# Performance work log

Measured on AMD Instinct MI355X. Metric: run time of the kernel, lower is better.

The kernel has to match this reference:

```python
import jax, jax.numpy as jnp
import numpy as np

NEG_INF = -1e32

def _linear(x, W, b):
    # torch nn.Linear: x @ W.T + b
    return x @ W.T + b

def setup_inputs() -> dict:
    key = jax.random.key(0)
    B, T, D, H = 8, 1024, 512, 8
    ks = jax.random.split(key, 16)
    def rn(i, shape, scale=1.0):
        return jax.random.normal(ks[i], shape, dtype=jnp.float32) * scale
    W_SCALE = 0.04  # ~xavier for 512x512
    inp = {
        'q_mean': rn(0, (B, T, D)), 'q_cov': rn(1, (B, T, D)),
        'k_mean': rn(2, (B, T, D)), 'k_cov': rn(3, (B, T, D)),
        'v_mean': rn(4, (B, T, D)), 'v_cov': rn(5, (B, T, D)),
        # kq_same=True: q projections share k weights
        'Wk_mean': rn(6, (D, D), W_SCALE), 'bk_mean': jnp.zeros((D,), jnp.float32),
        'Wk_cov':  rn(7, (D, D), W_SCALE), 'bk_cov':  jnp.zeros((D,), jnp.float32),
        'Wv_mean': rn(8, (D, D), W_SCALE), 'bv_mean': jnp.zeros((D,), jnp.float32),
        'Wv_cov':  rn(9, (D, D), W_SCALE), 'bv_cov':  jnp.zeros((D,), jnp.float32),
        'Wo_mean': rn(10, (D, D), W_SCALE), 'bo_mean': jnp.zeros((D,), jnp.float32),
        'Wo_cov':  rn(11, (D, D), W_SCALE), 'bo_cov':  jnp.zeros((D,), jnp.float32),
        'gammas': rn(12, (H, 1, 1), 0.3),
        'mask': jnp.broadcast_to(jnp.tril(jnp.ones((T, T), dtype=bool))[None, None], (B, 1, T, T)),
        'zero_pad': 1,
    }
    return inp

def reference(q_mean, q_cov, k_mean, k_cov, v_mean, v_cov,
              Wk_mean, bk_mean, Wk_cov, bk_cov,
              Wv_mean, bv_mean, Wv_cov, bv_cov,
              Wo_mean, bo_mean, Wo_cov, bo_cov,
              gammas, mask, zero_pad):
    B, T, D = q_mean.shape
    H = gammas.shape[0]
    dk = D // H
    def split(x):  # (B,T,D) -> (B,H,T,dk)
        return x.reshape(B, T, H, dk).transpose(0, 2, 1, 3)
    km = split(_linear(k_mean, Wk_mean, bk_mean))
    kc = split(_linear(k_cov,  Wk_cov,  bk_cov))
    qm = split(_linear(q_mean, Wk_mean, bk_mean))  # kq_same
    qc = split(_linear(q_cov,  Wk_cov,  bk_cov))
    vm = split(_linear(v_mean, Wv_mean, bv_mean))
    vc = split(_linear(v_cov,  Wv_cov,  bv_cov))

    # Wasserstein distance (B,H,T,T)
    m1sq = jnp.sum(qm ** 2, -1, keepdims=True)
    m2sq = jnp.sum(km ** 2, -1, keepdims=True)
    ret = -2.0 * jnp.einsum('bhtd,bhsd->bhts', qm, km) + m1sq + jnp.swapaxes(m2sq, -1, -2)
    sq_q = jnp.sqrt(jnp.clip(qc, 1e-24))
    sq_k = jnp.sqrt(jnp.clip(kc, 1e-24))
    cov_ret = (-2.0 * jnp.einsum('bhtd,bhsd->bhts', sq_q, sq_k)
               + jnp.sum(qc, -1, keepdims=True)
               + jnp.swapaxes(jnp.sum(kc, -1, keepdims=True), -1, -2))
    scores = -(ret + cov_ret) / jnp.sqrt(jnp.float32(dk))

    # cumulative position-decay term (no-grad block in torch)
    s_ = jnp.where(mask, scores, NEG_INF)
    s_ = jax.nn.softmax(s_, axis=-1) * mask.astype(scores.dtype)
    distcum = jnp.cumsum(s_, axis=-1)
    disttot = jnp.sum(s_, axis=-1, keepdims=True)
    idx = jnp.arange(T)
    pos = jnp.abs(idx[None, :] - idx[:, None]).astype(jnp.float32)[None, None]  # (1,1,T,T)
    dist_scores = jax.lax.stop_gradient(jnp.sqrt(jnp.clip((disttot - distcum) * pos, 0.0)))

    gamma = -jax.nn.softplus(gammas)[None]  # (1,H,1,1)
    total_effect = jnp.clip(jnp.exp(dist_scores * gamma), 1e-5, 1e5)
    scores = jnp.where(mask, scores * total_effect, NEG_INF)
    scores = jax.nn.softmax(scores, axis=-1)
    if zero_pad:
        scores = scores.at[:, :, 0, :].set(0.0)
    # dropout is identity (p=0 / eval)

    out_mean = jnp.einsum('bhts,bhsd->bhtd', scores, vm)
    out_cov  = jnp.einsum('bhts,bhsd->bhtd', scores ** 2, vc)
    cm = out_mean.transpose(0, 2, 1, 3).reshape(B, T, D)
    cc = out_cov.transpose(0, 2, 1, 3).reshape(B, T, D)
    return (_linear(cm, Wo_mean, bo_mean), _linear(cc, Wo_cov, bo_cov))
```

## Files before the change

kernel.cpp:

```cpp
#include <hip/hip_runtime.h>
#include <hip/hip_bf16.h>
#include <hip/hip_fp16.h>

#define Bb 8
#define Tt 1024
#define Dd 512
#define Hh 8

typedef _Float16 half8 __attribute__((ext_vector_type(8)));
typedef float floatx4 __attribute__((ext_vector_type(4)));

__device__ __forceinline__ half8 cvt8(float4 a, float4 b) {
    half8 h;
    h[0] = (_Float16)a.x; h[1] = (_Float16)a.y; h[2] = (_Float16)a.z; h[3] = (_Float16)a.w;
    h[4] = (_Float16)b.x; h[5] = (_Float16)b.y; h[6] = (_Float16)b.z; h[7] = (_Float16)b.w;
    return h;
}

__device__ __forceinline__ void async16(const _Float16* g, _Float16* l) {
    __builtin_amdgcn_global_load_lds(
        (const __attribute__((address_space(1))) uint32_t*)g,
        (__attribute__((address_space(3))) uint32_t*)l, 16, 0, 0);
}

#define DPP_ADD(v, ctrl) \
    ((v) + __int_as_float(__builtin_amdgcn_update_dpp(0, __float_as_int(v), (ctrl), 0xF, 0xF, true)))

__device__ __forceinline__ float red16(float v) {
    v = DPP_ADD(v, 0xB1);
    v = DPP_ADD(v, 0x4E);
    v = DPP_ADD(v, 0x141);
    v = DPP_ADD(v, 0x140);
    return v;
}
__device__ __forceinline__ float scan16(float v) {
    v = DPP_ADD(v, 0x111);
    v = DPP_ADD(v, 0x112);
    v = DPP_ADD(v, 0x114);
    v = DPP_ADD(v, 0x118);
    return v;
}

__global__ __launch_bounds__(256) void cvt_pre(
    const float* __restrict__ s0, const float* __restrict__ s1,
    const float* __restrict__ s2, const float* __restrict__ s3,
    const float* __restrict__ s4, const float* __restrict__ s5,
    const float* __restrict__ w0, const float* __restrict__ w1,
    const float* __restrict__ w2, const float* __restrict__ w3,
    const float* __restrict__ w4, const float* __restrict__ w5,
    _Float16* __restrict__ dst)
{
    const size_t N_BTD = (size_t)Bb * Tt * Dd;
    const size_t NX = 6 * N_BTD;
    const size_t total8 = (NX + 6 * 262144) / 8;
    size_t i = (size_t)blockIdx.x * 256 + threadIdx.x;
    const size_t stride = (size_t)gridDim.x * 256;
    for (; i < total8; i += stride) {
        const size_t e = i * 8;
        const float* src;
        size_t off;
        if (e < NX) {
            const int seg = (int)(e >> 22);
            off = e & (N_BTD - 1);
            src = (seg == 0) ? s0 : (seg == 1) ? s1 : (seg == 2) ? s2
                : (seg == 3) ? s3 : (seg == 4) ? s4 : s5;
        } else {
            const size_t we = e - NX;
            const int seg = (int)(we >> 18);
            off = we & 262143;
            src = (seg == 0) ? w0 : (seg == 1) ? w1 : (seg == 2) ? w2
                : (seg == 3) ? w3 : (seg == 4) ? w4 : w5;
        }
        float4 a = *(const float4*)(src + off);
        float4 b = *(const float4*)(src + off + 4);
        *(half8*)(dst + e) = cvt8(a, b);
    }
}

template<bool TR>
__device__ __forceinline__ void gemm_tile_h(
    const _Float16* __restrict__ X, const _Float16* __restrict__ W,
    _Float16* As, _Float16* Bs, int m0, int n0, floatx4 acc[8])
{
    const int tid = threadIdx.x;
    const int w = tid >> 6, lane = tid & 63;
    const int sl = lane & 15, quad = lane >> 4;
    const int j7 = tid & 7;
    const int swz = sl & 7;

    for (int k0 = 0; k0 < 512; k0 += 64) {
        #pragma unroll
        for (int i = 0; i < 2; i++) {
            const int slot = i * 256 + tid;
            const int row = slot >> 3;
            async16(X + (size_t)(m0 + row) * 512 + k0 + ((j7 ^ (row & 7)) << 3),
                    As + slot * 8);
        }
        #pragma unroll
        for (int i = 0; i < 4; i++) {
            const int slot = i * 256 + tid;
            const int row = slot >> 3;
            async16(W + (size_t)(n0 + row) * 512 + k0 + ((j7 ^ (row & 7)) << 3),
                    Bs + slot * 8);
        }
        __syncthreads();
        #pragma unroll
        for (int kc = 0; kc < 64; kc += 32) {
            const int jq = (kc >> 3) + quad;
            const half8 af = *(const half8*)(As + (w * 16 + sl) * 64 + ((jq ^ swz) << 3));
            #pragma unroll
            for (int tn = 0; tn < 8; tn++) {
                const half8 bf = *(const half8*)(Bs + (tn * 16 + sl) * 64 + ((jq ^ swz) << 3));
                if constexpr (TR)
                    acc[tn] = __builtin_amdgcn_mfma_f32_16x16x32_f16(bf, af, acc[tn], 0, 0, 0);
                else
                    acc[tn] = __builtin_amdgcn_mfma_f32_16x16x32_f16(af, bf, acc[tn], 0, 0, 0);
            }
        }
        __syncthreads();
    }
}

__global__ __launch_bounds__(256) void gemm6(
    const _Float16* __restrict__ XH, const _Float16* __restrict__ WH,
    const float* __restrict__ bk_mean, const float* __restrict__ bk_cov,
    const float* __restrict__ bv_mean, const float* __restrict__ bv_cov,
    _Float16* __restrict__ QB, _Float16* __restrict__ KB, _Float16* __restrict__ VB,
    float* __restrict__ RROW, float* __restrict__ CCOL)
{
    __shared__ __align__(16) _Float16 As[64 * 64];
    __shared__ __align__(16) _Float16 Bs[128 * 64];

    const int f = blockIdx.x;
    const int work = (f & 7) * 384 + (f >> 3);
    const int z = work >> 9;
    const int rem = work & 511;
    const int m0 = (rem >> 2) * 64;
    const int n0 = (rem & 3) * 128;

    const size_t N_BTD = (size_t)Bb * Tt * Dd;
    const _Float16* X = XH + (size_t)z * N_BTD;
    const _Float16* W;
    const float* bias;
    _Float16* outH; float* sums;
    int off, sumsq, do_sqrt;
    switch (z) {
    case 0:  W=WH;            bias=bk_mean; outH=QB; sums=RROW;   off=0;  sumsq=1; do_sqrt=0; break;
    case 1:  W=WH+262144;     bias=bk_cov;  outH=QB; sums=RROW;   off=64; sumsq=0; do_sqrt=1; break;
    case 2:  W=WH;            bias=bk_mean; outH=KB; sums=CCOL;   off=0;  sumsq=1; do_sqrt=0; break;
    case 3:  W=WH+262144;     bias=bk_cov;  outH=KB; sums=CCOL;   off=64; sumsq=0; do_sqrt=1; break;
    case 4:  W=WH+2*262144;   bias=bv_mean; outH=VB; sums=nullptr;off=0;  sumsq=0; do_sqrt=0; break;
    default: W=WH+3*262144;   bias=bv_cov;  outH=VB; sums=nullptr;off=64; sumsq=0; do_sqrt=0; break;
    }

    floatx4 acc[8];
    #pragma unroll
    for (int tn = 0; tn < 8; tn++) acc[tn] = (floatx4){0.f, 0.f, 0.f, 0.f};

    const int tid = threadIdx.x;
    const int w = tid >> 6, lane = tid & 63;
    const int sl = lane & 15, quad = lane >> 4;

    if (z < 4) {
        gemm_tile_h<false>(X, W, As, Bs, m0, n0, acc);
        #pragma unroll
        for (int r = 0; r < 4; r++) {
            const int m = m0 + w * 16 + quad * 4 + r;
            const int b = m >> 10, t = m & 1023;
            float rs0 = 0.f, rs1 = 0.f;
            #pragma unroll
            for (int tn = 0; tn < 8; tn++) {
                const int n = n0 + tn * 16 + sl;
                const float v = acc[tn][r] + bias[n];
                if (tn < 4) rs0 += sumsq ? v * v : v;
                else        rs1 += sumsq ? v * v : v;
                const float sv = do_sqrt ? sqrtf(fmaxf(v, 1e-24f)) : v;
                const int head = n >> 6, dd = n & 63;
                outH[(((size_t)b * Hh + head) * Tt + t) * 128 + off + dd] = (_Float16)sv;
            }
            if (sums) {
                float v0 = rs0, v1 = rs1;
                v0 += __shfl_xor(v0, 1); v0 += __shfl_xor(v0, 2);
                v0 += __shfl_xor(v0, 4); v0 += __shfl_xor(v0, 8);
                v1 += __shfl_xor(v1, 1); v1 += __shfl_xor(v1, 2);
                v1 += __shfl_xor(v1, 4); v1 += __shfl_xor(v1, 8);
                if (sl == 0) {
                    atomicAdd(&sums[((size_t)b * Hh + (n0 >> 6) + 0) * Tt + t], v0);
                    atomicAdd(&sums[((size_t)b * Hh + (n0 >> 6) + 1) * Tt + t], v1);
                }
            }
        }
    } else {
        gemm_tile_h<true>(X, W, As, Bs, m0, n0, acc);
        const int m = m0 + w * 16 + sl;
        const int b = m >> 10, t = m & 1023;
        #pragma unroll
        for (int r = 0; r < 4; r++) {
            #pragma unroll
            for (int tn = 0; tn < 8; tn++) {
                const int n = n0 + tn * 16 + quad * 4 + r;
                const float v = acc[tn][r] + bias[n];
                const int head = n >> 6, dd = n & 63;
                outH[(((size_t)b * Hh + head) * 128 + off + dd) * 1024 + t] = (_Float16)v;
            }
        }
    }
}

__global__ __launch_bounds__(256) void gemm_out(
    const _Float16* __restrict__ CMh, const _Float16* __restrict__ CCh,
    const _Float16* __restrict__ WH,
    const float* __restrict__ bo_mean, const float* __restrict__ bo_cov,
    float* __restrict__ out, size_t outStride)
{
    __shared__ __align__(16) _Float16 As[64 * 64];
    __shared__ __align__(16) _Float16 Bs[128 * 64];

    const int f = blockIdx.x;
    const int work = (f & 7) * 128 + (f >> 3);
    const int z = work >> 9;
    const int rem = work & 511;
    const int m0 = (rem >> 2) * 64;
    const int n0 = (rem & 3) * 128;

    const _Float16* X = z ? CCh : CMh;
    const _Float16* W = WH + (size_t)(4 + z) * 262144;
    const float* bias = z ? bo_cov : bo_mean;
    float* outF       = out + (size_t)z * outStride;

    floatx4 acc[8];
    #pragma unroll
    for (int tn = 0; tn < 8; tn++) acc[tn] = (floatx4){0.f, 0.f, 0.f, 0.f};
    gemm_tile_h<false>(X, W, As, Bs, m0, n0, acc);

    const int tid = threadIdx.x;
    const int w = tid >> 6, lane = tid & 63;
    const int sl = lane & 15, quad = lane >> 4;

    #pragma unroll
    for (int r = 0; r < 4; r++) {
        const int m = m0 + w * 16 + quad * 4 + r;
        #pragma unroll
        for (int tn = 0; tn < 8; tn++) {
            const int n = n0 + tn * 16 + sl;
            outF[(size_t)m * 512 + n] = acc[tn][r] + bias[n];
        }
    }
}

__global__ __launch_bounds__(256) void pass_a(
    const _Float16* __restrict__ QB, const _Float16* __restrict__ KB,
    const float* __restrict__ RROW, const float* __restrict__ CCOL,
    float* __restrict__ L1)
{
    const int tri = blockIdx.x;
    int rt = (int)((sqrtf(8.f * (float)tri + 1.f) - 1.f) * 0.5f);
    while ((rt + 1) * (rt + 2) / 2 <= tri) rt++;
    while (rt * (rt + 1) / 2 > tri) rt--;
    const int c = tri - rt * (rt + 1) / 2;
    const int bh = blockIdx.y;

    const int tid = threadIdx.x;
    const int w = tid >> 6, lane = tid & 63;
    const int sl = lane & 15, quad = lane >> 4;
    const int t0 = rt * 64;
    const int tbase = t0 + w * 16 + quad * 4;
    const size_t rowbase = (size_t)bh * Tt;

    half8 af[4];
    {
        const _Float16* qrow = QB + (rowbase + t0 + w * 16 + sl) * 128;
        #pragma unroll
        for (int ks = 0; ks < 4; ks++)
            af[ks] = *(const half8*)(qrow + ks * 32 + quad * 8);
    }
    float rt_[4];
    #pragma unroll
    for (int r = 0; r < 4; r++) rt_[r] = RROW[rowbase + tbase + r];

    const _Float16* KBb = KB + rowbase * 128;
    const float* CCb = CCOL + rowbase;

    float l1p[4] = {0.f, 0.f, 0.f, 0.f};
    #pragma unroll
    for (int su = 0; su < 4; su++) {
        const int scol = c * 64 + su * 16 + sl;
        const _Float16* kr = KBb + (size_t)scol * 128;
        floatx4 acc = {0.f, 0.f, 0.f, 0.f};
        #pragma unroll
        for (int ks = 0; ks < 4; ks++) {
            half8 bf = *(const half8*)(kr + ks * 32 + quad * 8);
            acc = __builtin_amdgcn_mfma_f32_16x16x32_f16(af[ks], bf, acc, 0, 0, 0);
        }
        const float cs = CCb[scol];
        #pragma unroll
        for (int r = 0; r < 4; r++) {
            const float S = 0.25f * acc[r] - 0.125f * (rt_[r] + cs);
            l1p[r] += (scol <= tbase + r) ? __expf(S) : 0.f;
        }
    }
    #pragma unroll
    for (int r = 0; r < 4; r++) {
        const float v = red16(l1p[r]);
        if (sl == 0) atomicAdd(&L1[rowbase + tbase + r], v);
    }
}

__global__ __launch_bounds__(256) void attn_b(
    const _Float16* __restrict__ QB, const _Float16* __restrict__ KB,
    const _Float16* __restrict__ VBt, const float* __restrict__ RROW,
    const float* __restrict__ CCOL, const float* __restrict__ L1,
    const float* __restrict__ gammas, const int* __restrict__ zp,
    _Float16* __restrict__ CMh, _Float16* __restrict__ CCh)
{
    __shared__ __align__(16) _Float16 Vt[2][128 * 64];
    __shared__ __align__(16) _Float16 Pm[4][16 * 64];

    const int tid = threadIdx.x;
    const int g = blockIdx.x >> 6;
    const int bh = blockIdx.x & 63;
    const int rt = (g < 8) ? (15 - g) : (g - 8);
    const int t0 = rt * 64;
    const int h = bh & 7, b = bh >> 3;
    const int w = tid >> 6, lane = tid & 63;
    const int sl = lane & 15, quad = lane >> 4;
    const size_t rowbase = (size_t)bh * Tt;
    const int nch = rt + 1;

    const _Float16* VBb = VBt + (size_t)bh * 128 * 1024;
    const int vr8 = tid >> 3;
    const int vc8 = (tid & 7) << 3;
    const int vswz = (vr8 & 7) << 3;
    const _Float16* vsrc0 = VBb + (size_t)vr8 * 1024 + (vc8 ^ vswz);
    #define STAGE_V(cc, buf) do {                                          \
        const _Float16* _s = vsrc0 + (cc) * 64;                            \
        _Float16* _d = &Vt[(buf)][0] + vr8 * 64 + vc8;                     \
        _Pragma("unroll")                                                  \
        for (int _i = 0; _i < 4; _i++)                                     \
            async16(_s + (size_t)_i * 32 * 1024, _d + _i * 32 * 64);       \
    } while (0)

    STAGE_V(0, 0);

    half8 af[4];
    {
        const _Float16* qrow = QB + (rowbase + t0 + w * 16 + sl) * 128;
        #pragma unroll
        for (int ks = 0; ks < 4; ks++)
            af[ks] = *(const half8*)(qrow + ks * 32 + quad * 8);
    }

    const float gamma = -log1pf(__expf(gammas[h]));
    const int zero_pad = *zp;
    const int tbase = t0 + w * 16 + quad * 4;

    float rt_[4], invl1[4];
    #pragma unroll
    for (int r = 0; r < 4; r++) {
        rt_[r] = RROW[rowbase + tbase + r];
        invl1[r] = 1.f / L1[rowbase + tbase + r];
    }

    const _Float16* KBb = KB + rowbase * 128;
    const float* CCb = CCOL + rowbase;

    __syncthreads();

    float cumc[4] = {0.f, 0.f, 0.f, 0.f};
    float runL2[4] = {0.f, 0.f, 0.f, 0.f};
    floatx4 accm[4], accc[4];
    #pragma unroll
    for (int nt = 0; nt < 4; nt++) {
        accm[nt] = (floatx4){0.f, 0.f, 0.f, 0.f};
        accc[nt] = (floatx4){0.f, 0.f, 0.f, 0.f};
    }
    _Float16* PmW = &Pm[w][0];

    for (int c = 0; c < nch; ++c) {
        const int cur = c & 1;
        if (c + 1 < nch) STAGE_V(c + 1, cur ^ 1);

        float p2v[4][4];
        float csum[4] = {0.f, 0.f, 0.f, 0.f};
        #pragma unroll
        for (int su = 0; su < 4; su++) {
            const int scol = c * 64 + su * 16 + sl;
            const _Float16* kr = KBb + (size_t)scol * 128;
            floatx4 acc = {0.f, 0.f, 0.f, 0.f};
            #pragma unroll
            for (int ks = 0; ks < 4; ks++) {
                half8 bf = *(const half8*)(kr + ks * 32 + quad * 8);
                acc = __builtin_amdgcn_mfma_f32_16x16x32_f16(af[ks], bf, acc, 0, 0, 0);
            }
            const float cs = CCb[scol];
            #pragma unroll
            for (int r = 0; r < 4; r++) {
                const bool valid = (scol <= tbase + r);
                const float S = 0.25f * acc[r] - 0.125f * (rt_[r] + cs);
                const float p1 = valid ? __expf(S) : 0.f;
                const float cum = cumc[r] + scan16(p1);
                cumc[r] += red16(p1);
                const float sn = 1.f - cum * invl1[r];
                const float dsq = sn * (float)(tbase + r - scol);
                const float dist = sqrtf(fmaxf(dsq, 0.f));
                float dec = __expf(gamma * dist);
                dec = fminf(fmaxf(dec, 1e-5f), 1e5f);
                const float p2 = valid ? __expf(S * dec) : 0.f;
                p2v[su][r] = p2;
                csum[r] += p2;
            }
        }

        float invL2c[4];
        #pragma unroll
        for (int r = 0; r < 4; r++) {
            const float v = red16(csum[r]);
            const float newL2 = runL2[r] + v;
            const float inv = 1.f / newL2;
            const float ratio = runL2[r] * inv;
            runL2[r] = newL2;
            invL2c[r] = inv;
            const float ratio2 = ratio * ratio;
            #pragma unroll
            for (int nt = 0; nt < 4; nt++) {
                accm[nt][r] *= ratio;
                accc[nt][r] *= ratio2;
            }
        }
        #pragma unroll
        for (int su = 0; su < 4; su++) {
            #pragma unroll
            for (int r = 0; r < 4; r++) {
                const float pn = p2v[su][r] * invL2c[r];
                const int prow = quad * 4 + r;
                PmW[prow * 64 + ((su * 16 + sl) ^ ((prow & 7) << 3))] = (_Float16)pn;
            }
        }

        const _Float16* Vc = &Vt[cur][0];
        #pragma unroll
        for (int ks = 0; ks < 2; ks++) {
            const int kb = ks * 32 + quad * 8;
            half8 am = *(const half8*)(PmW + sl * 64 + (kb ^ ((sl & 7) << 3)));
            half8 ac = am * am;
            #pragma unroll
            for (int nt = 0; nt < 4; nt++) {
                const int rm = nt * 16 + sl, rc = rm + 64;
                half8 bm = *(const half8*)(Vc + rm * 64 + (kb ^ ((rm & 7) << 3)));
                half8 bc = *(const half8*)(Vc + rc * 64 + (kb ^ ((rc & 7) << 3)));
                accm[nt] = __builtin_amdgcn_mfma_f32_16x16x32_f16(am, bm, accm[nt], 0, 0, 0);
                accc[nt] = __builtin_amdgcn_mfma_f32_16x16x32_f16(ac, bc, accc[nt], 0, 0, 0);
            }
        }
        __syncthreads();
    }

    #pragma unroll
    for (int r = 0; r < 4; r++) {
        const int t = tbase + r;
        const bool zr = (zero_pad && t == 0);
        _Float16* cmp = CMh + ((size_t)b * Tt + t) * Dd + h * 64;
        _Float16* ccp = CCh + ((size_t)b * Tt + t) * Dd + h * 64;
        #pragma unroll
        for (int nt = 0; nt < 4; nt++) {
            const int d = nt * 16 + sl;
            cmp[d] = (_Float16)(zr ? 0.f : accm[nt][r]);
            ccp[d] = (_Float16)(zr ? 0.f : accc[nt][r]);
        }
    }
    #undef STAGE_V
}

extern "C" void kernel_launch(void* const* d_in, const int* in_sizes, int n_in,
                              void* d_out, int out_size, void* d_ws, size_t ws_size,
                              hipStream_t stream)
{
    const float* q_mean  = (const float*)d_in[0];
    const float* q_cov   = (const float*)d_in[1];
    const float* k_mean  = (const float*)d_in[2];
    const float* k_cov   = (const float*)d_in[3];
    const float* v_mean  = (const float*)d_in[4];
    const float* v_cov   = (const float*)d_in[5];
    const float* Wk_mean = (const float*)d_in[6];
    const float* bk_mean = (const float*)d_in[7];
    const float* Wk_cov  = (const float*)d_in[8];
    const float* bk_cov  = (const float*)d_in[9];
    const float* Wv_mean = (const float*)d_in[10];
    const float* bv_mean = (const float*)d_in[11];
    const float* Wv_cov  = (const float*)d_in[12];
    const float* bv_cov  = (const float*)d_in[13];
    const float* Wo_mean = (const float*)d_in[14];
    const float* bo_mean = (const float*)d_in[15];
    const float* Wo_cov  = (const float*)d_in[16];
    const float* bo_cov  = (const float*)d_in[17];
    const float* gammas  = (const float*)d_in[18];
    const int* zero_pad  = (const int*)d_in[20];
    float* out = (float*)d_out;

    const size_t N_BHT128 = (size_t)Bb * Hh * Tt * 128;
    const size_t N_BHT    = (size_t)Bb * Hh * Tt;
    const size_t N_BTD    = (size_t)Bb * Tt * Dd;

    const size_t needed = 3 * N_BHT128 * sizeof(_Float16)
                        + 6 * N_BTD * sizeof(_Float16)
                        + 6 * 262144 * sizeof(_Float16)
                        + 3 * N_BHT * sizeof(float);
    if (ws_size < needed) return;

    _Float16* QB = (_Float16*)d_ws;
    _Float16* KB = QB + N_BHT128;
    _Float16* VB = KB + N_BHT128;
    _Float16* XH = VB + N_BHT128;
    _Float16* WH = XH + 6 * N_BTD;
    float* RROW = (float*)(WH + 6 * 262144);
    float* CCOL = RROW + N_BHT;
    float* L1   = CCOL + N_BHT;
    _Float16* CMh = XH;
    _Float16* CCh = CMh + N_BTD;

    hipMemsetAsync(RROW, 0, 3 * N_BHT * sizeof(float), stream);

    cvt_pre<<<dim3(2048), dim3(256), 0, stream>>>(
        q_mean, q_cov, k_mean, k_cov, v_mean, v_cov,
        Wk_mean, Wk_cov, Wv_mean, Wv_cov, Wo_mean, Wo_cov, XH);

    gemm6<<<dim3(3072), dim3(256), 0, stream>>>(
        XH, WH, bk_mean, bk_cov, bv_mean, bv_cov,
        QB, KB, VB, RROW, CCOL);

    pass_a<<<dim3(136, 64), dim3(256), 0, stream>>>(
        QB, KB, RROW, CCOL, L1);

    attn_b<<<dim3(1024), dim3(256), 0, stream>>>(
        QB, KB, VB, RROW, CCOL, L1, gammas, zero_pad, CMh, CCh);

    gemm_out<<<dim3(1024), dim3(256), 0, stream>>>(
        CMh, CCh, WH, bo_mean, bo_cov, out, N_BTD);
}
```

Before: 455.9 us.

## Enlarge GEMM tiles to 128x128 with 2x2 warp layout and coarsen pass_a blocks

The projection and output GEMMs move from 64x128 tiles with each warp owning 16 rows to 128x128 tiles where each warp computes a 64x64 sub-block (4x4 MFMA tiles). This reuses each LDS fragment load across more MFMAs and halves the number of blocks. pass_a now has each block process up to four 64-wide column tiles of a row tile instead of one, so fewer blocks and fewer atomics are needed. The cost is more accumulator registers, possibly lower occupancy, and a serial loop for the row-tile search in pass_a.

```diff
diff --git a/kernel.cpp b/kernel.cpp
--- a/kernel.cpp
+++ b/kernel.cpp
@@ -80,17 +80,18 @@
 template<bool TR>
 __device__ __forceinline__ void gemm_tile_h(
     const _Float16* __restrict__ X, const _Float16* __restrict__ W,
-    _Float16* As, _Float16* Bs, int m0, int n0, floatx4 acc[8])
+    _Float16* As, _Float16* Bs, int m0, int n0, floatx4 acc[4][4])
 {
     const int tid = threadIdx.x;
     const int w = tid >> 6, lane = tid & 63;
     const int sl = lane & 15, quad = lane >> 4;
+    const int wm = w >> 1, wn = w & 1;
     const int j7 = tid & 7;
     const int swz = sl & 7;
 
     for (int k0 = 0; k0 < 512; k0 += 64) {
         #pragma unroll
-        for (int i = 0; i < 2; i++) {
+        for (int i = 0; i < 4; i++) {
             const int slot = i * 256 + tid;
             const int row = slot >> 3;
             async16(X + (size_t)(m0 + row) * 512 + k0 + ((j7 ^ (row & 7)) << 3),
@@ -107,14 +108,22 @@
         #pragma unroll
         for (int kc = 0; kc < 64; kc += 32) {
             const int jq = (kc >> 3) + quad;
-            const half8 af = *(const half8*)(As + (w * 16 + sl) * 64 + ((jq ^ swz) << 3));
-            #pragma unroll
-            for (int tn = 0; tn < 8; tn++) {
-                const half8 bf = *(const half8*)(Bs + (tn * 16 + sl) * 64 + ((jq ^ swz) << 3));
-                if constexpr (TR)
-                    acc[tn] = __builtin_amdgcn_mfma_f32_16x16x32_f16(bf, af, acc[tn], 0, 0, 0);
-                else
-                    acc[tn] = __builtin_amdgcn_mfma_f32_16x16x32_f16(af, bf, acc[tn], 0, 0, 0);
+            half8 af[4], bf[4];
+            #pragma unroll
+            for (int mt = 0; mt < 4; mt++)
+                af[mt] = *(const half8*)(As + (wm * 64 + mt * 16 + sl) * 64 + ((jq ^ swz) << 3));
+            #pragma unroll
+            for (int nt = 0; nt < 4; nt++)
+                bf[nt] = *(const half8*)(Bs + (wn * 64 + nt * 16 + sl) * 64 + ((jq ^ swz) << 3));
+            #pragma unroll
+            for (int mt = 0; mt < 4; mt++) {
+                #pragma unroll
+                for (int nt = 0; nt < 4; nt++) {
+                    if constexpr (TR)
+                        acc[mt][nt] = __builtin_amdgcn_mfma_f32_16x16x32_f16(bf[nt], af[mt], acc[mt][nt], 0, 0, 0);
+                    else
+                        acc[mt][nt] = __builtin_amdgcn_mfma_f32_16x16x32_f16(af[mt], bf[nt], acc[mt][nt], 0, 0, 0);
+                }
             }
         }
         __syncthreads();
@@ -128,15 +137,15 @@
     _Float16* __restrict__ QB, _Float16* __restrict__ KB, _Float16* __restrict__ VB,
     float* __restrict__ RROW, float* __restrict__ CCOL)
 {
-    __shared__ __align__(16) _Float16 As[64 * 64];
+    __shared__ __align__(16) _Float16 As[128 * 64];
     __shared__ __align__(16) _Float16 Bs[128 * 64];
 
     const int f = blockIdx.x;
-    const int work = (f & 7) * 384 + (f >> 3);
-    const int z = work >> 9;
-    const int rem = work & 511;
-    const int m0 = (rem >> 2) * 64;
-    const int n0 = (rem & 3) * 128;
+    const int work = (f & 7) * 192 + (f >> 3);
+    const int z = work >> 8;
+    const int rem = work & 255;
+    const int m0 = (rem >> 2) << 7;
+    const int n0 = (rem & 3) << 7;
 
     const size_t N_BTD = (size_t)Bb * Tt * Dd;
     const _Float16* X = XH + (size_t)z * N_BTD;
@@ -153,55 +162,58 @@
     default: W=WH+3*262144;   bias=bv_cov;  outH=VB; sums=nullptr;off=64; sumsq=0; do_sqrt=0; break;
     }
 
-    floatx4 acc[8];
-    #pragma unroll
-    for (int tn = 0; tn < 8; tn++) acc[tn] = (floatx4){0.f, 0.f, 0.f, 0.f};
+    floatx4 acc[4][4];
+    #pragma unroll
+    for (int mt = 0; mt < 4; mt++)
+        #pragma unroll
+        for (int nt = 0; nt < 4; nt++)
+            acc[mt][nt] = (floatx4){0.f, 0.f, 0.f, 0.f};
 
     const int tid = threadIdx.x;
     const int w = tid >> 6, lane = tid & 63;
     const int sl = lane & 15, quad = lane >> 4;
+    const int wm = w >> 1, wn = w & 1;
 
     if (z < 4) {
         gemm_tile_h<false>(X, W, As, Bs, m0, n0, acc);
         #pragma unroll
-        for (int r = 0; r < 4; r++) {
-            const int m = m0 + w * 16 + quad * 4 + r;
-            const int b = m >> 10, t = m & 1023;
-            float rs0 = 0.f, rs1 = 0.f;
-            #pragma unroll
-            for (int tn = 0; tn < 8; tn++) {
-                const int n = n0 + tn * 16 + sl;
-                const float v = acc[tn][r] + bias[n];
-                if (tn < 4) rs0 += sumsq ? v * v : v;
-                else        rs1 += sumsq ? v * v : v;
-                const float sv = do_sqrt ? sqrtf(fmaxf(v, 1e-24f)) : v;
-                const int head = n >> 6, dd = n & 63;
-                outH[(((size_t)b * Hh + head) * Tt + t) * 128 + off + dd] = (_Float16)sv;
-            }
-            if (sums) {
-                float v0 = rs0, v1 = rs1;
-                v0 += __shfl_xor(v0, 1); v0 += __shfl_xor(v0, 2);
-                v0 += __shfl_xor(v0, 4); v0 += __shfl_xor(v0, 8);
-                v1 += __shfl_xor(v1, 1); v1 += __shfl_xor(v1, 2);
-                v1 += __shfl_xor(v1, 4); v1 += __shfl_xor(v1, 8);
-                if (sl == 0) {
-                    atomicAdd(&sums[((size_t)b * Hh + (n0 >> 6) + 0) * Tt + t], v0);
-                    atomicAdd(&sums[((size_t)b * Hh + (n0 >> 6) + 1) * Tt + t], v1);
+        for (int mt = 0; mt < 4; mt++) {
+            #pragma unroll
+            for (int r = 0; r < 4; r++) {
+                const int m = m0 + wm * 64 + mt * 16 + quad * 4 + r;
+                const int b = m >> 10, t = m & 1023;
+                float rs = 0.f;
+                #pragma unroll
+                for (int nt = 0; nt < 4; nt++) {
+                    const int n = n0 + wn * 64 + nt * 16 + sl;
+                    const float v = acc[mt][nt][r] + bias[n];
+                    rs += sumsq ? v * v : v;
+                    const float sv = do_sqrt ? sqrtf(fmaxf(v, 1e-24f)) : v;
+                    const int head = n >> 6, dd = n & 63;
+                    outH[(((size_t)b * Hh + head) * Tt + t) * 128 + off + dd] = (_Float16)sv;
+                }
+                if (sums) {
+                    const float v0 = red16(rs);
+                    if (sl == 0)
+                        atomicAdd(&sums[((size_t)b * Hh + (n0 >> 6) + wn) * Tt + t], v0);
                 }
             }
         }
     } else {
         gemm_tile_h<true>(X, W, As, Bs, m0, n0, acc);
-        const int m = m0 + w * 16 + sl;
-        const int b = m >> 10, t = m & 1023;
-        #pragma unroll
-        for (int r = 0; r < 4; r++) {
-            #pragma unroll
-            for (int tn = 0; tn < 8; tn++) {
-                const int n = n0 + tn * 16 + quad * 4 + r;
-                const float v = acc[tn][r] + bias[n];
-                const int head = n >> 6, dd = n & 63;
-                outH[(((size_t)b * Hh + head) * 128 + off + dd) * 1024 + t] = (_Float16)v;
+        #pragma unroll
+        for (int mt = 0; mt < 4; mt++) {
+            const int m = m0 + wm * 64 + mt * 16 + sl;
+            const int b = m >> 10, t = m & 1023;
+            #pragma unroll
+            for (int nt = 0; nt < 4; nt++) {
+                #pragma unroll
+                for (int r = 0; r < 4; r++) {
+                    const int n = n0 + wn * 64 + nt * 16 + quad * 4 + r;
+                    const float v = acc[mt][nt][r] + bias[n];
+                    const int head = n >> 6, dd = n & 63;
+                    outH[(((size_t)b * Hh + head) * 128 + off + dd) * 1024 + t] = (_Float16)v;
+                }
             }
         }
     }
@@ -213,37 +225,44 @@
     const float* __restrict__ bo_mean, const float* __restrict__ bo_cov,
     float* __restrict__ out, size_t outStride)
 {
-    __shared__ __align__(16) _Float16 As[64 * 64];
+    __shared__ __align__(16) _Float16 As[128 * 64];
     __shared__ __align__(16) _Float16 Bs[128 * 64];
 
     const int f = blockIdx.x;
-    const int work = (f & 7) * 128 + (f >> 3);
-    const int z = work >> 9;
-    const int rem = work & 511;
-    const int m0 = (rem >> 2) * 64;
-    const int n0 = (rem & 3) * 128;
+    const int work = (f & 7) * 64 + (f >> 3);
+    const int z = work >> 8;
+    const int rem = work & 255;
+    const int m0 = (rem >> 2) << 7;
+    const int n0 = (rem & 3) << 7;
 
     const _Float16* X = z ? CCh : CMh;
     const _Float16* W = WH + (size_t)(4 + z) * 262144;
     const float* bias = z ? bo_cov : bo_mean;
     float* outF       = out + (size_t)z * outStride;
 
-    floatx4 acc[8];
-    #pragma unroll
-    for (int tn = 0; tn < 8; tn++) acc[tn] = (floatx4){0.f, 0.f, 0.f, 0.f};
+    floatx4 acc[4][4];
+    #pragma unroll
+    for (int mt = 0; mt < 4; mt++)
+        #pragma unroll
+        for (int nt = 0; nt < 4; nt++)
+            acc[mt][nt] = (floatx4){0.f, 0.f, 0.f, 0.f};
     gemm_tile_h<false>(X, W, As, Bs, m0, n0, acc);
 
     const int tid = threadIdx.x;
     const int w = tid >> 6, lane = tid & 63;
     const int sl = lane & 15, quad = lane >> 4;
-
-    #pragma unroll
-    for (int r = 0; r < 4; r++) {
-        const int m = m0 + w * 16 + quad * 4 + r;
-        #pragma unroll
-        for (int tn = 0; tn < 8; tn++) {
-            const int n = n0 + tn * 16 + sl;
-            outF[(size_t)m * 512 + n] = acc[tn][r] + bias[n];
+    const int wm = w >> 1, wn = w & 1;
+
+    #pragma unroll
+    for (int mt = 0; mt < 4; mt++) {
+        #pragma unroll
+        for (int r = 0; r < 4; r++) {
+            const int m = m0 + wm * 64 + mt * 16 + quad * 4 + r;
+            #pragma unroll
+            for (int nt = 0; nt < 4; nt++) {
+                const int n = n0 + wn * 64 + nt * 16 + sl;
+                outF[(size_t)m * 512 + n] = acc[mt][nt][r] + bias[n];
+            }
         }
     }
 }
@@ -253,11 +272,11 @@
     const float* __restrict__ RROW, const float* __restrict__ CCOL,
     float* __restrict__ L1)
 {
-    const int tri = blockIdx.x;
-    int rt = (int)((sqrtf(8.f * (float)tri + 1.f) - 1.f) * 0.5f);
-    while ((rt + 1) * (rt + 2) / 2 <= tri) rt++;
-    while (rt * (rt + 1) / 2 > tri) rt--;
-    const int c = tri - rt * (rt + 1) / 2;
+    const int gi = blockIdx.x;
+    int rt = 0, cum = 0;
+    while (cum + ((rt + 4) >> 2) <= gi) { cum += (rt + 4) >> 2; rt++; }
+    const int c0 = (gi - cum) * 4;
+    const int cend = min(c0 + 4, rt + 1);
     const int bh = blockIdx.y;
 
     const int tid = threadIdx.x;
@@ -282,21 +301,23 @@
     const float* CCb = CCOL + rowbase;
 
     float l1p[4] = {0.f, 0.f, 0.f, 0.f};
-    #pragma unroll
-    for (int su = 0; su < 4; su++) {
-        const int scol = c * 64 + su * 16 + sl;
-        const _Float16* kr = KBb + (size_t)scol * 128;
-        floatx4 acc = {0.f, 0.f, 0.f, 0.f};
-        #pragma unroll
-        for (int ks = 0; ks < 4; ks++) {
-            half8 bf = *(const half8*)(kr + ks * 32 + quad * 8);
-            acc = __builtin_amdgcn_mfma_f32_16x16x32_f16(af[ks], bf, acc, 0, 0, 0);
-        }
-        const float cs = CCb[scol];
-        #pragma unroll
-        for (int r = 0; r < 4; r++) {
-            const float S = 0.25f * acc[r] - 0.125f * (rt_[r] + cs);
-            l1p[r] += (scol <= tbase + r) ? __expf(S) : 0.f;
+    for (int c = c0; c < cend; ++c) {
+        #pragma unroll
+        for (int su = 0; su < 4; su++) {
+            const int scol = c * 64 + su * 16 + sl;
+            const _Float16* kr = KBb + (size_t)scol * 128;
+            floatx4 acc = {0.f, 0.f, 0.f, 0.f};
+            #pragma unroll
+            for (int ks = 0; ks < 4; ks++) {
+                half8 bf = *(const half8*)(kr + ks * 32 + quad * 8);
+                acc = __builtin_amdgcn_mfma_f32_16x16x32_f16(af[ks], bf, acc, 0, 0, 0);
+            }
+            const float cs = CCb[scol];
+            #pragma unroll
+            for (int r = 0; r < 4; r++) {
+                const float S = 0.25f * acc[r] - 0.125f * (rt_[r] + cs);
+                l1p[r] += (scol <= tbase + r) ? __expf(S) : 0.f;
+            }
         }
     }
     #pragma unroll
@@ -524,16 +545,16 @@
         q_mean, q_cov, k_mean, k_cov, v_mean, v_cov,
         Wk_mean, Wk_cov, Wv_mean, Wv_cov, Wo_mean, Wo_cov, XH);
 
-    gemm6<<<dim3(3072), dim3(256), 0, stream>>>(
+    gemm6<<<dim3(1536), dim3(256), 0, stream>>>(
         XH, WH, bk_mean, bk_cov, bv_mean, bv_cov,
         QB, KB, VB, RROW, CCOL);
 
-    pass_a<<<dim3(136, 64), dim3(256), 0, stream>>>(
+    pass_a<<<dim3(40, 64), dim3(256), 0, stream>>>(
         QB, KB, RROW, CCOL, L1);
 
     attn_b<<<dim3(1024), dim3(256), 0, stream>>>(
         QB, KB, VB, RROW, CCOL, L1, gammas, zero_pad, CMh, CCh);
 
-    gemm_out<<<dim3(1024), dim3(256), 0, stream>>>(
+    gemm_out<<<dim3(512), dim3(256), 0, stream>>>(
         CMh, CCh, WH, bo_mean, bo_cov, out, N_BTD);
 }
```

Result: slower. 466.3 us (+2.3%).
